# Kernel optimization log

Hardware: AMD Instinct MI355X
Metric: run time of the kernel (lower is better)

## Reference

```python
import jax, jax.numpy as jnp
import numpy as np

H = 4  # heads


def _tconv(x, src, dst, ea, Wq, bq, Wk, bk, Wv, bv, We, Ws, bs):
    # PyG TransformerConv, heads=4, concat=False, root_weight=True, beta=False
    N = x.shape[0]
    Dh = Wq.shape[1] // H  # per-head dim (= hidden_channels)
    q = (x @ Wq + bq).reshape(N, H, Dh)
    k = (x @ Wk + bk).reshape(N, H, Dh)
    v = (x @ Wv + bv).reshape(N, H, Dh)
    e = (ea @ We).reshape(-1, H, Dh)      # lin_edge has no bias in PyG
    kj = k[src] + e                        # [E, H, Dh]
    vj = v[src] + e                        # [E, H, Dh]
    alpha = (q[dst] * kj).sum(-1) / jnp.sqrt(jnp.asarray(Dh, x.dtype))  # [E, H]
    # segment softmax over incoming edges of each dst node
    m = jax.ops.segment_max(alpha, dst, num_segments=N)
    a = jnp.exp(alpha - m[dst])
    s = jax.ops.segment_sum(a, dst, num_segments=N)
    a = a / (s[dst] + 1e-16)
    out = jax.ops.segment_sum(a[:, :, None] * vj, dst, num_segments=N)  # [N, H, Dh]
    out = out.mean(axis=1)                 # concat=False -> mean over heads
    return out + x @ Ws + bs               # root/skip connection


def setup_inputs() -> dict:
    key = jax.random.key(0)
    ks = jax.random.split(key, 32)
    N, E, C_in, C_e, Ch = 50000, 800000, 32, 16, 32
    d = {}
    d['x'] = jax.random.normal(ks[0], (N, C_in), dtype=jnp.float32)
    d['edge_attr'] = jax.random.normal(ks[1], (E, C_e), dtype=jnp.float32)
    d['edge_index'] = jax.random.randint(ks[2], (2, E), 0, N, dtype=jnp.int32)
    s = 0.05
    i = 3
    for L, cin in ((1, C_in), (2, Ch)):
        d[f'Wq{L}'] = jax.random.normal(ks[i], (cin, H * Ch)) * s; i += 1
        d[f'bq{L}'] = jnp.zeros((H * Ch,), jnp.float32)
        d[f'Wk{L}'] = jax.random.normal(ks[i], (cin, H * Ch)) * s; i += 1
        d[f'bk{L}'] = jnp.zeros((H * Ch,), jnp.float32)
        d[f'Wv{L}'] = jax.random.normal(ks[i], (cin, H * Ch)) * s; i += 1
        d[f'bv{L}'] = jnp.zeros((H * Ch,), jnp.float32)
        d[f'We{L}'] = jax.random.normal(ks[i], (C_e, H * Ch)) * s; i += 1
        d[f'Ws{L}'] = jax.random.normal(ks[i], (cin, Ch)) * s; i += 1
        d[f'bs{L}'] = jnp.zeros((Ch,), jnp.float32)
    d['Wm1'] = jax.random.normal(ks[i], (2 * Ch + C_e, Ch)) * s; i += 1
    d['bm1'] = jnp.zeros((Ch,), jnp.float32)
    d['Wm2'] = jax.random.normal(ks[i], (Ch, 1)) * s; i += 1
    d['bm2'] = jnp.zeros((1,), jnp.float32)
    return d


def reference(x, edge_attr, edge_index,
              Wq1, bq1, Wk1, bk1, Wv1, bv1, We1, Ws1, bs1,
              Wq2, bq2, Wk2, bk2, Wv2, bv2, We2, Ws2, bs2,
              Wm1, bm1, Wm2, bm2):
    src, dst = edge_index[0], edge_index[1]
    h = jax.nn.relu(_tconv(x, src, dst, edge_attr, Wq1, bq1, Wk1, bk1, Wv1, bv1, We1, Ws1, bs1))
    h = jax.nn.relu(_tconv(h, src, dst, edge_attr, Wq2, bq2, Wk2, bk2, Wv2, bv2, We2, Ws2, bs2))
    ef = jnp.concatenate([h[src], edge_attr, h[dst]], axis=-1)  # [E, 2*Ch + C_e]
    out = jax.nn.relu(ef @ Wm1 + bm1) @ Wm2 + bm2
    return out.reshape(-1)
```

## Files before the change

### kernel.cpp

```cpp
#include <hip/hip_runtime.h>
#include <hip/hip_fp16.h>
#include <math.h>

#define D128 128
#define CH32 32
#define CE16 16

__global__ void k_hist(const int* __restrict__ dst, int* __restrict__ deg, int E) {
    int e = blockIdx.x * blockDim.x + threadIdx.x;
    if (e < E) atomicAdd(&deg[dst[e]], 1);
}

__global__ void k_scan1(const int* __restrict__ deg, int* __restrict__ offs,
                        int* __restrict__ bsum, int N) {
    __shared__ int buf[256];
    int t = threadIdx.x;
    int i = blockIdx.x * 256 + t;
    int v = (i < N) ? deg[i] : 0;
    buf[t] = v;
    __syncthreads();
    #pragma unroll
    for (int off = 1; off < 256; off <<= 1) {
        int val = (t >= off) ? buf[t - off] : 0;
        __syncthreads();
        buf[t] += val;
        __syncthreads();
    }
    if (i < N) offs[i] = buf[t] - v;
    if (t == 255) bsum[blockIdx.x] = buf[255];
}

__global__ void k_scan2(const int* __restrict__ bsum, int* __restrict__ boff, int nb) {
    __shared__ int buf[256];
    int t = threadIdx.x;
    int v = (t < nb) ? bsum[t] : 0;
    buf[t] = v;
    __syncthreads();
    #pragma unroll
    for (int off = 1; off < 256; off <<= 1) {
        int val = (t >= off) ? buf[t - off] : 0;
        __syncthreads();
        buf[t] += val;
        __syncthreads();
    }
    if (t < nb) boff[t] = buf[t] - v;
}

__global__ void k_scan3(const int* __restrict__ boff, int* __restrict__ offs,
                        int* __restrict__ cur, int N, int E) {
    int i = blockIdx.x * blockDim.x + threadIdx.x;
    if (i < N) {
        int o = offs[i] + boff[i >> 8];
        offs[i] = o;
        cur[i] = o;
    }
    if (i == 0) offs[N] = E;
}

__global__ void k_scatter(const int* __restrict__ src, const int* __restrict__ dst,
                          int* __restrict__ cur, int* __restrict__ csr_srcb,
                          float4* __restrict__ ea_csr4, const float4* __restrict__ ea4,
                          int E) {
    int e = blockIdx.x * blockDim.x + threadIdx.x;
    if (e < E) {
        int d = dst[e];
        int p = atomicAdd(&cur[d], 1);
        csr_srcb[p] = src[e] << 9;
        float4 a0 = ea4[e * 4 + 0];
        float4 a1 = ea4[e * 4 + 1];
        float4 a2 = ea4[e * 4 + 2];
        float4 a3 = ea4[e * 4 + 3];
        ea_csr4[p * 4 + 0] = a0;
        ea_csr4[p * 4 + 1] = a1;
        ea_csr4[p * 4 + 2] = a2;
        ea_csr4[p * 4 + 3] = a3;
    }
}

__global__ __launch_bounds__(128) void k_nodeproj(
    const float* __restrict__ xin,
    const float* __restrict__ Wq, const float* __restrict__ bq,
    const float* __restrict__ Wk, const float* __restrict__ bk,
    const float* __restrict__ Wv, const float* __restrict__ bv,
    const float* __restrict__ Ws, const float* __restrict__ bs,
    float* __restrict__ q, __half* __restrict__ kvh,
    float* __restrict__ skip, int N)
{
    int tid = threadIdx.x;
    int c   = tid & 31;
    int pos = ((tid >> 2) << 3) | (tid & 3);
    float wq[32], wk[32], wv[32], ws[32];
    #pragma unroll
    for (int j = 0; j < 32; j++) {
        wq[j] = Wq[j * D128 + tid];
        wk[j] = Wk[j * D128 + tid];
        wv[j] = Wv[j * D128 + tid];
        ws[j] = Ws[j * CH32 + c];
    }
    float bqc = bq[tid], bkc = bk[tid], bvc = bv[tid], bsc = bs[c];
    __shared__ float xs[4][32];
    int nchunk = (N + 3) / 4;
    for (int chk = blockIdx.x; chk < nchunk; chk += gridDim.x) {
        int base = chk * 4;
        {
            int r = tid >> 5;
            int n = base + r;
            xs[r][c] = (n < N) ? xin[n * 32 + c] : 0.f;
        }
        __syncthreads();
        #pragma unroll
        for (int r = 0; r < 4; r++) {
            int n = base + r;
            if (n < N) {
                float aq = bqc, ak = bkc, av = bvc;
                #pragma unroll
                for (int j = 0; j < 32; j++) {
                    float xj = xs[r][j];
                    aq = fmaf(xj, wq[j], aq);
                    ak = fmaf(xj, wk[j], ak);
                    av = fmaf(xj, wv[j], av);
                }
                q[n * D128 + tid] = aq;
                kvh[(size_t)n * 256 + pos]     = __float2half_rn(ak);
                kvh[(size_t)n * 256 + pos + 4] = __float2half_rn(av);
            }
        }
        {
            int r = tid >> 5;
            int n = base + r;
            if (n < N) {
                float as = bsc;
                #pragma unroll
                for (int j = 0; j < 32; j++) as = fmaf(xs[r][j], ws[j], as);
                skip[n * 32 + c] = as;
            }
        }
        __syncthreads();
    }
}

__global__ __launch_bounds__(64) void k_edgeattn(
    const float* __restrict__ q, const __half* __restrict__ kvh,
    const float* __restrict__ skip,
    const float* __restrict__ ea_csr, const float* __restrict__ We,
    const int* __restrict__ offs, const int* __restrict__ csr_srcb,
    float* __restrict__ hout)
{
    int node = blockIdx.x;
    int lane = threadIdx.x;
    int eg   = lane >> 5;
    int c    = lane & 31;
    int g    = c & 7;
    int c4   = c << 2;

    const float QS = 0.17677669529663687f * 1.4426950408889634f;
    float4 qv = *(const float4*)&q[(size_t)node * D128 + c4];
    qv.x *= QS; qv.y *= QS; qv.z *= QS; qv.w *= QS;

    float qe0 = 0.f, qe1 = 0.f;
    #pragma unroll
    for (int j = 0; j < 16; j++) {
        float4 wj = *(const float4*)&We[j * D128 + c4];
        float t = fmaf(qv.w, wj.w, fmaf(qv.z, wj.z, fmaf(qv.y, wj.y, qv.x * wj.x)));
        t += __shfl_xor(t, 1);
        t += __shfl_xor(t, 2);
        t += __shfl_xor(t, 4);
        if (g == (j >> 1)) { if (j & 1) qe1 = t; else qe0 = t; }
    }

    int s0 = offs[node], s1 = offs[node + 1];
    int deg = s1 - s0;

    float l = 0.f;
    float ac0 = 0.f, ac1 = 0.f, ac2 = 0.f, ac3 = 0.f;
    float se0 = 0.f, se1 = 0.f;

    if (deg > 0) {
        int last = s1 - 1;
        const char* kvb = (const char*)kvh;
        int toff = c << 4;

        auto eidx = [&](int p) { return min(s0 + 2 * p + eg, last); };
        auto ldidx = [&](int p) { return csr_srcb[eidx(p)]; };
        auto ldkv  = [&](int ib) {
            return *(const float4*)(kvb + (size_t)(unsigned)ib + toff);
        };
        auto ldea  = [&](int p) {
            return *(const float2*)&ea_csr[(size_t)eidx(p) * 16 + 2 * g];
        };
        auto pair = [&](const float4& kvr, const float2& eav, int p) {
            bool valid = (s0 + 2 * p + eg) <= last;
            float2 k01 = __half22float2(*(const __half2*)&kvr.x);
            float2 k23 = __half22float2(*(const __half2*)&kvr.y);
            float2 v01 = __half22float2(*(const __half2*)&kvr.z);
            float2 v23 = __half22float2(*(const __half2*)&kvr.w);
            float t = fmaf(qv.y, k01.y, qv.x * k01.x);
            t = fmaf(qv.z, k23.x, t);
            t = fmaf(qv.w, k23.y, t);
            t = fmaf(qe0, eav.x, t);
            t = fmaf(qe1, eav.y, t);
            t += __shfl_xor(t, 1);
            t += __shfl_xor(t, 2);
            t += __shfl_xor(t, 4);
            float pp = valid ? __builtin_amdgcn_exp2f(t) : 0.f;
            l += pp;
            ac0 = fmaf(pp, v01.x, ac0);
            ac1 = fmaf(pp, v01.y, ac1);
            ac2 = fmaf(pp, v23.x, ac2);
            ac3 = fmaf(pp, v23.y, ac3);
            se0 = fmaf(pp, eav.x, se0);
            se1 = fmaf(pp, eav.y, se1);
        };

        int iA0 = ldidx(0), iA1 = ldidx(1);
        int iB0 = ldidx(2), iB1 = ldidx(3);
        float4 kA0 = ldkv(iA0), kA1 = ldkv(iA1);
        float2 eA0 = ldea(0),   eA1 = ldea(1);

        int p = 0;
        int nIter = (deg + 7) >> 3;
        for (int it = 0; it < nIter; ++it) {
            float4 kB0 = ldkv(iB0), kB1 = ldkv(iB1);
            float2 eB0 = ldea(p + 2), eB1 = ldea(p + 3);
            iA0 = ldidx(p + 4); iA1 = ldidx(p + 5);

            pair(kA0, eA0, p + 0);
            pair(kA1, eA1, p + 1);

            kA0 = ldkv(iA0); kA1 = ldkv(iA1);
            eA0 = ldea(p + 4); eA1 = ldea(p + 5);
            iB0 = ldidx(p + 6); iB1 = ldidx(p + 7);

            pair(kB0, eB0, p + 2);
            pair(kB1, eB1, p + 3);

            p += 4;
        }
    }

    asm volatile("" ::: "memory");

    l   += __shfl_xor(l, 32);
    ac0 += __shfl_xor(ac0, 32);
    ac1 += __shfl_xor(ac1, 32);
    ac2 += __shfl_xor(ac2, 32);
    ac3 += __shfl_xor(ac3, 32);
    se0 += __shfl_xor(se0, 32);
    se1 += __shfl_xor(se1, 32);

    float inv = 1.0f / (l + 1e-16f);
    float r0 = ac0 * inv, r1 = ac1 * inv, r2 = ac2 * inv, r3 = ac3 * inv;
    float sn0 = se0 * inv, sn1 = se1 * inv;

    int gb = lane & ~7;
    #pragma unroll
    for (int j = 0; j < 16; j++) {
        float sj = __shfl((j & 1) ? sn1 : sn0, gb | (j >> 1), 64);
        float4 wj = *(const float4*)&We[j * D128 + c4];
        r0 = fmaf(sj, wj.x, r0);
        r1 = fmaf(sj, wj.y, r1);
        r2 = fmaf(sj, wj.z, r2);
        r3 = fmaf(sj, wj.w, r3);
    }
    r0 += __shfl_xor(r0, 8);  r0 += __shfl_xor(r0, 16);
    r1 += __shfl_xor(r1, 8);  r1 += __shfl_xor(r1, 16);
    r2 += __shfl_xor(r2, 8);  r2 += __shfl_xor(r2, 16);
    r3 += __shfl_xor(r3, 8);  r3 += __shfl_xor(r3, 16);
    if (lane < 8) {
        const float4 sk = *(const float4*)&skip[(size_t)node * 32 + c4];
        float4 o;
        o.x = fmaxf(fmaf(0.25f, r0, sk.x), 0.f);
        o.y = fmaxf(fmaf(0.25f, r1, sk.y), 0.f);
        o.z = fmaxf(fmaf(0.25f, r2, sk.z), 0.f);
        o.w = fmaxf(fmaf(0.25f, r3, sk.w), 0.f);
        *(float4*)&hout[(size_t)node * 32 + c4] = o;
    }
}

__global__ __launch_bounds__(256) void k_mlp(
    const float* __restrict__ h, const float* __restrict__ ea,
    const int* __restrict__ src, const int* __restrict__ dst,
    const float* __restrict__ Wm1, const float* __restrict__ bm1,
    const float* __restrict__ Wm2, const float* __restrict__ bm2,
    float* __restrict__ out, int E)
{
    __shared__ float4 W4[80 * 8];
    __shared__ float bm1L[32];
    __shared__ float wm2L[32];
    int tid = threadIdx.x;
    const float4* Wm1_4 = (const float4*)Wm1;
    for (int i = tid; i < 640; i += 256) W4[i] = Wm1_4[i];
    if (tid < 32) { bm1L[tid] = bm1[tid]; wm2L[tid] = Wm2[tid]; }
    __syncthreads();

    int e = blockIdx.x * 256 + tid;
    if (e >= E) return;
    float b2 = bm2[0];
    int s = src[e], d = dst[e];

    float4 acc[8];
    #pragma unroll
    for (int i = 0; i < 8; i++) acc[i] = make_float4(0.f, 0.f, 0.f, 0.f);

    auto dorow = [&](int j, float xj) {
        #pragma unroll
        for (int c4 = 0; c4 < 8; c4++) {
            float4 w = W4[j * 8 + c4];
            acc[c4].x = fmaf(xj, w.x, acc[c4].x);
            acc[c4].y = fmaf(xj, w.y, acc[c4].y);
            acc[c4].z = fmaf(xj, w.z, acc[c4].z);
            acc[c4].w = fmaf(xj, w.w, acc[c4].w);
        }
    };

    const float4* hs  = (const float4*)(h + (size_t)s * 32);
    const float4* hd  = (const float4*)(h + (size_t)d * 32);
    const float4* eav = (const float4*)(ea + (size_t)e * 16);
    #pragma unroll
    for (int qd = 0; qd < 8; qd++) {
        float4 xv = hs[qd];
        dorow(qd * 4 + 0, xv.x); dorow(qd * 4 + 1, xv.y);
        dorow(qd * 4 + 2, xv.z); dorow(qd * 4 + 3, xv.w);
    }
    #pragma unroll
    for (int qd = 0; qd < 4; qd++) {
        float4 xv = eav[qd];
        dorow(32 + qd * 4 + 0, xv.x); dorow(32 + qd * 4 + 1, xv.y);
        dorow(32 + qd * 4 + 2, xv.z); dorow(32 + qd * 4 + 3, xv.w);
    }
    #pragma unroll
    for (int qd = 0; qd < 8; qd++) {
        float4 xv = hd[qd];
        dorow(48 + qd * 4 + 0, xv.x); dorow(48 + qd * 4 + 1, xv.y);
        dorow(48 + qd * 4 + 2, xv.z); dorow(48 + qd * 4 + 3, xv.w);
    }

    float y = b2;
    #pragma unroll
    for (int c4 = 0; c4 < 8; c4++) {
        y += fmaxf(acc[c4].x + bm1L[c4 * 4 + 0], 0.f) * wm2L[c4 * 4 + 0];
        y += fmaxf(acc[c4].y + bm1L[c4 * 4 + 1], 0.f) * wm2L[c4 * 4 + 1];
        y += fmaxf(acc[c4].z + bm1L[c4 * 4 + 2], 0.f) * wm2L[c4 * 4 + 2];
        y += fmaxf(acc[c4].w + bm1L[c4 * 4 + 3], 0.f) * wm2L[c4 * 4 + 3];
    }
    out[e] = y;
}

extern "C" void kernel_launch(void* const* d_in, const int* in_sizes, int n_in,
                              void* d_out, int out_size, void* d_ws, size_t ws_size,
                              hipStream_t stream)
{
    const float* x  = (const float*)d_in[0];
    const float* ea = (const float*)d_in[1];
    const int*   ei = (const int*)d_in[2];
    const int N = in_sizes[0] / 32;
    const int E = in_sizes[1] / 16;
    const int* src = ei;
    const int* dst = ei + E;

    const float *Wq1 = (const float*)d_in[3],  *bq1 = (const float*)d_in[4];
    const float *Wk1 = (const float*)d_in[5],  *bk1 = (const float*)d_in[6];
    const float *Wv1 = (const float*)d_in[7],  *bv1 = (const float*)d_in[8];
    const float *We1 = (const float*)d_in[9],  *Ws1 = (const float*)d_in[10];
    const float *bs1 = (const float*)d_in[11];
    const float *Wq2 = (const float*)d_in[12], *bq2 = (const float*)d_in[13];
    const float *Wk2 = (const float*)d_in[14], *bk2 = (const float*)d_in[15];
    const float *Wv2 = (const float*)d_in[16], *bv2 = (const float*)d_in[17];
    const float *We2 = (const float*)d_in[18], *Ws2 = (const float*)d_in[19];
    const float *bs2 = (const float*)d_in[20];
    const float *Wm1 = (const float*)d_in[21], *bm1 = (const float*)d_in[22];
    const float *Wm2 = (const float*)d_in[23], *bm2 = (const float*)d_in[24];

    char* w = (char*)d_ws;
    auto alloc = [&](size_t bytes) -> void* {
        void* p = (void*)w;
        w += (bytes + 255) & ~(size_t)255;
        return p;
    };
    int* deg      = (int*)alloc((size_t)N * 4);
    int* offs     = (int*)alloc(((size_t)N + 1) * 4);
    int* cur      = (int*)alloc((size_t)N * 4);
    int* bsum     = (int*)alloc(256 * 4);
    int* boff     = (int*)alloc(256 * 4);
    int* csr_srcb = (int*)alloc((size_t)E * 4);
    float* ea_csr = (float*)alloc((size_t)E * 16 * 4);
    float* qb     = (float*)alloc((size_t)N * 128 * 4);
    __half* kvb   = (__half*)alloc((size_t)N * 256 * 2);
    float* skipb  = (float*)alloc((size_t)N * 32 * 4);
    float* h1     = (float*)alloc((size_t)N * 32 * 4);
    float* h2     = (float*)alloc((size_t)N * 32 * 4);

    hipMemsetAsync(deg, 0, (size_t)N * 4, stream);

    int ebl = (E + 255) / 256;
    int nb  = (N + 255) / 256;
    k_hist<<<ebl, 256, 0, stream>>>(dst, deg, E);
    k_scan1<<<nb, 256, 0, stream>>>(deg, offs, bsum, N);
    k_scan2<<<1, 256, 0, stream>>>(bsum, boff, nb);
    k_scan3<<<nb, 256, 0, stream>>>(boff, offs, cur, N, E);
    k_scatter<<<ebl, 256, 0, stream>>>(src, dst, cur, csr_srcb,
                                       (float4*)ea_csr, (const float4*)ea, E);

    k_nodeproj<<<1024, 128, 0, stream>>>(x, Wq1, bq1, Wk1, bk1, Wv1, bv1, Ws1, bs1,
                                         qb, kvb, skipb, N);
    k_edgeattn<<<N, 64, 0, stream>>>(qb, kvb, skipb, ea_csr, We1,
                                     offs, csr_srcb, h1);
    k_nodeproj<<<1024, 128, 0, stream>>>(h1, Wq2, bq2, Wk2, bk2, Wv2, bv2, Ws2, bs2,
                                         qb, kvb, skipb, N);
    k_edgeattn<<<N, 64, 0, stream>>>(qb, kvb, skipb, ea_csr, We2,
                                     offs, csr_srcb, h2);
    k_mlp<<<ebl, 256, 0, stream>>>(h2, ea, src, dst, Wm1, bm1, Wm2, bm2,
                                   (float*)d_out, E);
}
```

Measured before the change: 542.9 us.

## Precompute q·We per node and factor MLP first layer into node projections

Adds a small kernel that folds Wq and We into a combined 32x64 matrix, plus a per-node projection kernel that computes the q-dot-edge-weight terms ahead of time, so the attention kernel no longer runs the 16-iteration shuffle reduction per node. The edge MLP's first layer is split algebraically: h[src]·WA+bias and h[dst]·WC are computed once per node in a new postproj kernel, leaving only the 16-wide edge_attr product per edge. This cuts per-edge FLOPs from 80x32 to 16x32 and per-node attention prologue work. In exchange it adds extra launches and extra node-sized buffers to read and write.

```diff
diff --git a/kernel.cpp b/kernel.cpp
--- a/kernel.cpp
+++ b/kernel.cpp
@@ -77,6 +77,56 @@
     }
 }
 
+__global__ void k_wqe(const float* __restrict__ Wq, const float* __restrict__ bq,
+                      const float* __restrict__ We,
+                      float* __restrict__ Wqe, float* __restrict__ bqe) {
+    int t = threadIdx.x;
+    int h = t >> 4, j = t & 15;
+    const float QS = 0.17677669529663687f * 1.4426950408889634f;
+    float wecol[32];
+    #pragma unroll
+    for (int d = 0; d < 32; d++) wecol[d] = We[j * D128 + h * 32 + d];
+    for (int i = 0; i < 32; i++) {
+        float s = 0.f;
+        #pragma unroll
+        for (int d = 0; d < 32; d++) s = fmaf(Wq[i * D128 + h * 32 + d], wecol[d], s);
+        Wqe[i * 64 + t] = s * QS;
+    }
+    float s = 0.f;
+    #pragma unroll
+    for (int d = 0; d < 32; d++) s = fmaf(bq[h * 32 + d], wecol[d], s);
+    bqe[t] = s * QS;
+}
+
+__global__ __launch_bounds__(256) void k_qeproj(
+    const float* __restrict__ x, const float* __restrict__ Wqe,
+    const float* __restrict__ bqe, float* __restrict__ qeb, int N) {
+    __shared__ float W[32][64];
+    __shared__ float xs[4][32];
+    int tid = threadIdx.x;
+    for (int i = tid; i < 32 * 64; i += 256) W[i >> 6][i & 63] = Wqe[i];
+    int col = tid & 63, r = tid >> 6;
+    float b = bqe[col];
+    __syncthreads();
+    int nchunk = (N + 3) / 4;
+    for (int chk = blockIdx.x; chk < nchunk; chk += gridDim.x) {
+        int n = chk * 4 + r;
+        if (tid < 128) {
+            int rr = tid >> 5, cc = tid & 31;
+            int nn = chk * 4 + rr;
+            xs[rr][cc] = (nn < N) ? x[nn * 32 + cc] : 0.f;
+        }
+        __syncthreads();
+        if (n < N) {
+            float a = b;
+            #pragma unroll
+            for (int j = 0; j < 32; j++) a = fmaf(xs[r][j], W[j][col], a);
+            qeb[(size_t)n * 64 + col] = a;
+        }
+        __syncthreads();
+    }
+}
+
 __global__ __launch_bounds__(128) void k_nodeproj(
     const float* __restrict__ xin,
     const float* __restrict__ Wq, const float* __restrict__ bq,
@@ -144,7 +194,7 @@
     const float* __restrict__ skip,
     const float* __restrict__ ea_csr, const float* __restrict__ We,
     const int* __restrict__ offs, const int* __restrict__ csr_srcb,
-    float* __restrict__ hout)
+    const float* __restrict__ qeb, float* __restrict__ hout)
 {
     int node = blockIdx.x;
     int lane = threadIdx.x;
@@ -157,16 +207,8 @@
     float4 qv = *(const float4*)&q[(size_t)node * D128 + c4];
     qv.x *= QS; qv.y *= QS; qv.z *= QS; qv.w *= QS;
 
-    float qe0 = 0.f, qe1 = 0.f;
-    #pragma unroll
-    for (int j = 0; j < 16; j++) {
-        float4 wj = *(const float4*)&We[j * D128 + c4];
-        float t = fmaf(qv.w, wj.w, fmaf(qv.z, wj.z, fmaf(qv.y, wj.y, qv.x * wj.x)));
-        t += __shfl_xor(t, 1);
-        t += __shfl_xor(t, 2);
-        t += __shfl_xor(t, 4);
-        if (g == (j >> 1)) { if (j & 1) qe1 = t; else qe0 = t; }
-    }
+    float2 qe01 = *(const float2*)&qeb[(size_t)node * 64 + ((c >> 3) << 4) + 2 * g];
+    float qe0 = qe01.x, qe1 = qe01.y;
 
     int s0 = offs[node], s1 = offs[node + 1];
     int deg = s1 - s0;
@@ -238,8 +280,6 @@
         }
     }
 
-    asm volatile("" ::: "memory");
-
     l   += __shfl_xor(l, 32);
     ac0 += __shfl_xor(ac0, 32);
     ac1 += __shfl_xor(ac1, 32);
@@ -277,20 +317,53 @@
     }
 }
 
+__global__ __launch_bounds__(256) void k_postproj(
+    const float* __restrict__ h, const float* __restrict__ Wm1,
+    const float* __restrict__ bm1, float* __restrict__ hA,
+    float* __restrict__ hC, int N) {
+    __shared__ float WA[32][32], WC[32][32];
+    __shared__ float hs[8][32];
+    int tid = threadIdx.x;
+    for (int i = tid; i < 1024; i += 256) {
+        WA[i >> 5][i & 31] = Wm1[i];
+        WC[i >> 5][i & 31] = Wm1[48 * 32 + i];
+    }
+    int col = tid & 31, r = tid >> 5;
+    float bb = bm1[col];
+    __syncthreads();
+    int nchunk = (N + 7) / 8;
+    for (int chk = blockIdx.x; chk < nchunk; chk += gridDim.x) {
+        int n = chk * 8 + r;
+        hs[r][col] = (n < N) ? h[(size_t)n * 32 + col] : 0.f;
+        __syncthreads();
+        if (n < N) {
+            float a = bb, cc = 0.f;
+            #pragma unroll
+            for (int j = 0; j < 32; j++) {
+                float hj = hs[r][j];
+                a  = fmaf(hj, WA[j][col], a);
+                cc = fmaf(hj, WC[j][col], cc);
+            }
+            hA[(size_t)n * 32 + col] = a;
+            hC[(size_t)n * 32 + col] = cc;
+        }
+        __syncthreads();
+    }
+}
+
 __global__ __launch_bounds__(256) void k_mlp(
-    const float* __restrict__ h, const float* __restrict__ ea,
+    const float* __restrict__ hA, const float* __restrict__ hC,
+    const float* __restrict__ ea,
     const int* __restrict__ src, const int* __restrict__ dst,
-    const float* __restrict__ Wm1, const float* __restrict__ bm1,
-    const float* __restrict__ Wm2, const float* __restrict__ bm2,
-    float* __restrict__ out, int E)
+    const float* __restrict__ Wm1, const float* __restrict__ Wm2,
+    const float* __restrict__ bm2, float* __restrict__ out, int E)
 {
-    __shared__ float4 W4[80 * 8];
-    __shared__ float bm1L[32];
+    __shared__ float4 B4[16 * 8];
     __shared__ float wm2L[32];
     int tid = threadIdx.x;
-    const float4* Wm1_4 = (const float4*)Wm1;
-    for (int i = tid; i < 640; i += 256) W4[i] = Wm1_4[i];
-    if (tid < 32) { bm1L[tid] = bm1[tid]; wm2L[tid] = Wm2[tid]; }
+    const float4* Wm1B = (const float4*)(Wm1 + 32 * 32);
+    for (int i = tid; i < 128; i += 256) B4[i] = Wm1B[i];
+    if (tid < 32) wm2L[tid] = Wm2[tid];
     __syncthreads();
 
     int e = blockIdx.x * 256 + tid;
@@ -298,14 +371,21 @@
     float b2 = bm2[0];
     int s = src[e], d = dst[e];
 
+    const float4* pa  = (const float4*)(hA + (size_t)s * 32);
+    const float4* pc  = (const float4*)(hC + (size_t)d * 32);
+    const float4* eav = (const float4*)(ea + (size_t)e * 16);
+
     float4 acc[8];
     #pragma unroll
-    for (int i = 0; i < 8; i++) acc[i] = make_float4(0.f, 0.f, 0.f, 0.f);
+    for (int i = 0; i < 8; i++) {
+        float4 va = pa[i], vc = pc[i];
+        acc[i] = make_float4(va.x + vc.x, va.y + vc.y, va.z + vc.z, va.w + vc.w);
+    }
 
     auto dorow = [&](int j, float xj) {
         #pragma unroll
         for (int c4 = 0; c4 < 8; c4++) {
-            float4 w = W4[j * 8 + c4];
+            float4 w = B4[j * 8 + c4];
             acc[c4].x = fmaf(xj, w.x, acc[c4].x);
             acc[c4].y = fmaf(xj, w.y, acc[c4].y);
             acc[c4].z = fmaf(xj, w.z, acc[c4].z);
@@ -313,35 +393,20 @@
         }
     };
 
-    const float4* hs  = (const float4*)(h + (size_t)s * 32);
-    const float4* hd  = (const float4*)(h + (size_t)d * 32);
-    const float4* eav = (const float4*)(ea + (size_t)e * 16);
-    #pragma unroll
-    for (int qd = 0; qd < 8; qd++) {
-        float4 xv = hs[qd];
+    #pragma unroll
+    for (int qd = 0; qd < 4; qd++) {
+        float4 xv = eav[qd];
         dorow(qd * 4 + 0, xv.x); dorow(qd * 4 + 1, xv.y);
         dorow(qd * 4 + 2, xv.z); dorow(qd * 4 + 3, xv.w);
     }
-    #pragma unroll
-    for (int qd = 0; qd < 4; qd++) {
-        float4 xv = eav[qd];
-        dorow(32 + qd * 4 + 0, xv.x); dorow(32 + qd * 4 + 1, xv.y);
-        dorow(32 + qd * 4 + 2, xv.z); dorow(32 + qd * 4 + 3, xv.w);
-    }
-    #pragma unroll
-    for (int qd = 0; qd < 8; qd++) {
-        float4 xv = hd[qd];
-        dorow(48 + qd * 4 + 0, xv.x); dorow(48 + qd * 4 + 1, xv.y);
-        dorow(48 + qd * 4 + 2, xv.z); dorow(48 + qd * 4 + 3, xv.w);
-    }
 
     float y = b2;
     #pragma unroll
     for (int c4 = 0; c4 < 8; c4++) {
-        y += fmaxf(acc[c4].x + bm1L[c4 * 4 + 0], 0.f) * wm2L[c4 * 4 + 0];
-        y += fmaxf(acc[c4].y + bm1L[c4 * 4 + 1], 0.f) * wm2L[c4 * 4 + 1];
-        y += fmaxf(acc[c4].z + bm1L[c4 * 4 + 2], 0.f) * wm2L[c4 * 4 + 2];
-        y += fmaxf(acc[c4].w + bm1L[c4 * 4 + 3], 0.f) * wm2L[c4 * 4 + 3];
+        y += fmaxf(acc[c4].x, 0.f) * wm2L[c4 * 4 + 0];
+        y += fmaxf(acc[c4].y, 0.f) * wm2L[c4 * 4 + 1];
+        y += fmaxf(acc[c4].z, 0.f) * wm2L[c4 * 4 + 2];
+        y += fmaxf(acc[c4].w, 0.f) * wm2L[c4 * 4 + 3];
     }
     out[e] = y;
 }
@@ -389,6 +454,13 @@
     float* skipb  = (float*)alloc((size_t)N * 32 * 4);
     float* h1     = (float*)alloc((size_t)N * 32 * 4);
     float* h2     = (float*)alloc((size_t)N * 32 * 4);
+    float* Wqe1   = (float*)alloc(32 * 64 * 4);
+    float* bqe1   = (float*)alloc(64 * 4);
+    float* Wqe2   = (float*)alloc(32 * 64 * 4);
+    float* bqe2   = (float*)alloc(64 * 4);
+    float* qeb    = (float*)alloc((size_t)N * 64 * 4);
+    float* hA     = (float*)alloc((size_t)N * 32 * 4);
+    float* hC     = (float*)alloc((size_t)N * 32 * 4);
 
     hipMemsetAsync(deg, 0, (size_t)N * 4, stream);
 
@@ -400,15 +472,20 @@
     k_scan3<<<nb, 256, 0, stream>>>(boff, offs, cur, N, E);
     k_scatter<<<ebl, 256, 0, stream>>>(src, dst, cur, csr_srcb,
                                        (float4*)ea_csr, (const float4*)ea, E);
+    k_wqe<<<1, 64, 0, stream>>>(Wq1, bq1, We1, Wqe1, bqe1);
+    k_wqe<<<1, 64, 0, stream>>>(Wq2, bq2, We2, Wqe2, bqe2);
 
     k_nodeproj<<<1024, 128, 0, stream>>>(x, Wq1, bq1, Wk1, bk1, Wv1, bv1, Ws1, bs1,
                                          qb, kvb, skipb, N);
+    k_qeproj<<<1024, 256, 0, stream>>>(x, Wqe1, bqe1, qeb, N);
     k_edgeattn<<<N, 64, 0, stream>>>(qb, kvb, skipb, ea_csr, We1,
-                                     offs, csr_srcb, h1);
+                                     offs, csr_srcb, qeb, h1);
     k_nodeproj<<<1024, 128, 0, stream>>>(h1, Wq2, bq2, Wk2, bk2, Wv2, bv2, Ws2, bs2,
                                          qb, kvb, skipb, N);
+    k_qeproj<<<1024, 256, 0, stream>>>(h1, Wqe2, bqe2, qeb, N);
     k_edgeattn<<<N, 64, 0, stream>>>(qb, kvb, skipb, ea_csr, We2,
-                                     offs, csr_srcb, h2);
-    k_mlp<<<ebl, 256, 0, stream>>>(h2, ea, src, dst, Wm1, bm1, Wm2, bm2,
+                                     offs, csr_srcb, qeb, h2);
+    k_postproj<<<1024, 256, 0, stream>>>(h2, Wm1, bm1, hA, hC, N);
+    k_mlp<<<ebl, 256, 0, stream>>>(hA, hC, ea, src, dst, Wm1, Wm2, bm2,
                                    (float*)d_out, E);
 }
```

Result: slower. 558.4 us (+2.9%).
